# Kernel tuning notes

Hardware: AMD Instinct MI355X
Metric: run time of the kernel (lower is better)

## Reference

```python
import jax, jax.numpy as jnp
import numpy as np

D = 512        # latent_dim
DT = 256       # text_latent_dim
H = 8          # num_heads
TE = 2048      # time_embed_dim
NEG = -1000000.0


def _ln(x, g, b, eps=1e-5):
    m = jnp.mean(x, axis=-1, keepdims=True)
    v = jnp.mean(jnp.square(x - m), axis=-1, keepdims=True)
    return (x - m) * jax.lax.rsqrt(v + eps) * g + b


def _linear(x, W, b):
    return x @ W.T + b


def setup_inputs() -> dict:
    key = jax.random.key(0)
    ks = jax.random.split(key, 24)
    B, T, NT, R, LR = 32, 1024, 77, 4, 256
    inp = {
        'x': jax.random.normal(ks[0], (B, T, D), jnp.float32),
        'xf': jax.random.normal(ks[1], (B, NT, DT), jnp.float32),
        'emb': jax.random.normal(ks[2], (B, TE), jnp.float32),
        'src_mask': jax.random.randint(ks[3], (B, T, 1), 0, 2).astype(jnp.float32),
        'cond_type': jax.random.randint(ks[4], (B, 1, 1), 0, 100).astype(jnp.int32),
        're_motion': jax.random.normal(ks[5], (B, R, LR, D), jnp.float32),
        're_text': jax.random.normal(ks[6], (B, R, 1, D), jnp.float32),
        're_mask': jax.random.randint(ks[7], (B, R, LR), 0, 2).astype(jnp.float32),
    }
    s = 0.02
    def W(k, o, i):
        return jax.random.normal(k, (o, i), jnp.float32) * s
    params = {
        'norm_g': jnp.ones((D,), jnp.float32), 'norm_b': jnp.zeros((D,), jnp.float32),
        'tnorm_g': jnp.ones((DT,), jnp.float32), 'tnorm_b': jnp.zeros((DT,), jnp.float32),
        'rn1_g': jnp.ones((2 * D,), jnp.float32), 'rn1_b': jnp.zeros((2 * D,), jnp.float32),
        'rn2_g': jnp.ones((D,), jnp.float32), 'rn2_b': jnp.zeros((D,), jnp.float32),
        'Wq': W(ks[8], D, D), 'bq': jnp.zeros((D,), jnp.float32),
        'Wkt': W(ks[9], D, DT), 'bkt': jnp.zeros((D,), jnp.float32),
        'Wvt': W(ks[10], D, DT), 'bvt': jnp.zeros((D,), jnp.float32),
        'Wkm': W(ks[11], D, D), 'bkm': jnp.zeros((D,), jnp.float32),
        'Wvm': W(ks[12], D, D), 'bvm': jnp.zeros((D,), jnp.float32),
        'Wkr': W(ks[13], D, 2 * D), 'bkr': jnp.zeros((D,), jnp.float32),
        'Wvr': W(ks[14], D, D), 'bvr': jnp.zeros((D,), jnp.float32),
        'emb_W': W(ks[15], 2 * D, TE), 'emb_b': jnp.zeros((2 * D,), jnp.float32),
        'snorm_g': jnp.ones((D,), jnp.float32), 'snorm_b': jnp.zeros((D,), jnp.float32),
        'out_W': W(ks[16], D, D), 'out_b': jnp.zeros((D,), jnp.float32),
    }
    inp.update(params)
    return inp


def _forward(x, xf, emb, src_mask, cond_type, re_motion, re_text, re_mask,
             norm_g, norm_b, tnorm_g, tnorm_b, rn1_g, rn1_b, rn2_g, rn2_b,
             Wq, bq, Wkt, bkt, Wvt, bvt, Wkm, bkm, Wvm, bvm, Wkr, bkr, Wvr, bvr,
             emb_W, emb_b, snorm_g, snorm_b, out_W, out_b):
    B, T, _ = x.shape
    re_mask_r = re_mask.reshape(B, -1, 1)                       # [B, R*LR, 1]
    N = xf.shape[1] + T + re_motion.shape[1] * re_motion.shape[2]

    xn = _ln(x, norm_g, norm_b)                                  # [B,T,D]
    xfn = _ln(xf, tnorm_g, tnorm_b)                              # [B,NT,DT]
    query = _linear(xn, Wq, bq)                                  # [B,T,D]

    text_ct = (cond_type % 10 > 0).astype(x.dtype)               # [B,1,1]
    retr_ct = (cond_type // 10 > 0).astype(x.dtype)              # [B,1,1]

    re_text_rep = jnp.broadcast_to(re_text, re_motion.shape)     # repeat along Lr
    re_feat_key = jnp.concatenate([re_motion, re_text_rep], axis=-1).reshape(B, -1, 2 * D)

    k_text = _linear(xfn, Wkt, bkt) + (1.0 - text_ct) * NEG
    k_retr = (_linear(_ln(re_feat_key, rn1_g, rn1_b), Wkr, bkr)
              + (1.0 - retr_ct) * NEG + (1.0 - re_mask_r) * NEG)
    k_mot = _linear(xn, Wkm, bkm) + (1.0 - src_mask) * NEG
    key_cat = jnp.concatenate([k_text, k_retr, k_mot], axis=1)   # [B,N,D]

    q = jax.nn.softmax(query.reshape(B, T, H, -1), axis=-1)      # softmax over head_dim
    k = jax.nn.softmax(key_cat.reshape(B, N, H, -1), axis=1)     # softmax over tokens

    re_feat_value = re_motion.reshape(B, -1, D)
    v_text = _linear(xfn, Wvt, bvt) * text_ct
    v_retr = _linear(_ln(re_feat_value, rn2_g, rn2_b), Wvr, bvr) * retr_ct * re_mask_r
    v_mot = _linear(xn, Wvm, bvm) * src_mask
    v = jnp.concatenate([v_text, v_retr, v_mot], axis=1).reshape(B, N, H, -1)

    attention = jnp.einsum('bnhd,bnhl->bhdl', k, v)              # [B,H,hd,hd]
    y = jnp.einsum('bthd,bhdl->bthl', q, attention).reshape(B, T, D)

    # StylizationBlock: film-style scale/shift from time embedding, zero-init out proj
    emb_out = _linear(jax.nn.silu(emb), emb_W, emb_b)[:, None, :]  # [B,1,2D]
    scale, shift = emb_out[..., :D], emb_out[..., D:]
    h = _ln(y, snorm_g, snorm_b) * (1.0 + scale) + shift
    h = _linear(jax.nn.silu(h), out_W, out_b)
    return x + h


def reference(x, xf, emb, src_mask, cond_type, re_motion, re_text, re_mask,
              norm_g, norm_b, tnorm_g, tnorm_b, rn1_g, rn1_b, rn2_g, rn2_b,
              Wq, bq, Wkt, bkt, Wvt, bvt, Wkm, bkm, Wvm, bvm, Wkr, bkr, Wvr, bvr,
              emb_W, emb_b, snorm_g, snorm_b, out_W, out_b):
    return _forward(x, xf, emb, src_mask, cond_type, re_motion, re_text, re_mask,
                    norm_g, norm_b, tnorm_g, tnorm_b, rn1_g, rn1_b, rn2_g, rn2_b,
                    Wq, bq, Wkt, bkt, Wvt, bvt, Wkm, bkm, Wvm, bvm, Wkr, bkr, Wvr, bvr,
                    emb_W, emb_b, snorm_g, snorm_b, out_W, out_b)
```

## Files before the change

### kernel.cpp

```cpp
#include <hip/hip_runtime.h>
#include <cstddef>
#include <cstdint>

#define DEV __device__ __forceinline__

namespace {

constexpr int kH = 8;
constexpr int kB = 32, kT = 1024, kNT = 77, kR = 4, kLR = 256;
constexpr int kRL = kR * kLR;
constexpr int kN = kNT + kRL + kT;
constexpr float kNEG = -1000000.0f;
constexpr int kNS = 8;
constexpr int kSL = 272;
constexpr int kLDSW = 136;

typedef __bf16 bf16x8 __attribute__((ext_vector_type(8)));
typedef float f32x4 __attribute__((ext_vector_type(4)));

DEV unsigned short f2bf(float f) {
  unsigned int u = __float_as_uint(f);
  u += 0x7fffu + ((u >> 16) & 1u);
  return (unsigned short)(u >> 16);
}
DEV float bf2f(unsigned short h) { return __uint_as_float(((unsigned int)h) << 16); }

DEV float wave_sum(float v) {
  #pragma unroll
  for (int s = 32; s; s >>= 1) v += __shfl_xor(v, s);
  return v;
}

template<int COLS>
__global__ __launch_bounds__(256) void ln_bf16(const float* __restrict__ in,
    const float* __restrict__ g, const float* __restrict__ be,
    unsigned short* __restrict__ out) {
  constexpr int PT = COLS / 256;
  int row = blockIdx.x;
  const float* p = in + (size_t)row * COLS;
  unsigned short* o = out + (size_t)row * COLS;
  float v[PT]; float s = 0.f, s2 = 0.f;
  #pragma unroll
  for (int i = 0; i < PT; i++) {
    v[i] = p[threadIdx.x + i * 256];
    s += v[i]; s2 += v[i] * v[i];
  }
  __shared__ float red[2][4];
  int lane = threadIdx.x & 63, w = threadIdx.x >> 6;
  s = wave_sum(s); s2 = wave_sum(s2);
  if (!lane) { red[0][w] = s; red[1][w] = s2; }
  __syncthreads();
  s = red[0][0] + red[0][1] + red[0][2] + red[0][3];
  s2 = red[1][0] + red[1][1] + red[1][2] + red[1][3];
  float mean = s / COLS;
  float var = s2 / COLS - mean * mean;
  float rstd = rsqrtf(var + 1e-5f);
  #pragma unroll
  for (int i = 0; i < PT; i++) {
    int c = threadIdx.x + i * 256;
    o[c] = f2bf((v[i] - mean) * rstd * g[c] + be[c]);
  }
}

__global__ __launch_bounds__(256) void rfk_norm(const float* __restrict__ mot,
    const float* __restrict__ txt,
    const float* __restrict__ g1, const float* __restrict__ b1,
    const float* __restrict__ g2, const float* __restrict__ b2,
    unsigned short* __restrict__ rfk, unsigned short* __restrict__ rfv) {
  int m = blockIdx.x;
  const float* pm = mot + (size_t)m * 512;
  const float* pt = txt + (size_t)(m >> 8) * 512;
  float v[2], t[2];
  float sv = 0.f, sv2 = 0.f, st = 0.f, st2 = 0.f;
  #pragma unroll
  for (int i = 0; i < 2; i++) {
    v[i] = pm[threadIdx.x + i * 256]; sv += v[i]; sv2 += v[i] * v[i];
    t[i] = pt[threadIdx.x + i * 256]; st += t[i]; st2 += t[i] * t[i];
  }
  __shared__ float red[4][4];
  int lane = threadIdx.x & 63, w = threadIdx.x >> 6;
  sv = wave_sum(sv); sv2 = wave_sum(sv2); st = wave_sum(st); st2 = wave_sum(st2);
  if (!lane) { red[0][w] = sv; red[1][w] = sv2; red[2][w] = st; red[3][w] = st2; }
  __syncthreads();
  float SV = red[0][0] + red[0][1] + red[0][2] + red[0][3];
  float SV2 = red[1][0] + red[1][1] + red[1][2] + red[1][3];
  float ST = red[2][0] + red[2][1] + red[2][2] + red[2][3];
  float ST2 = red[3][0] + red[3][1] + red[3][2] + red[3][3];
  float SA = SV + ST, SA2 = SV2 + ST2;
  float ma = SA / 1024.f, va = SA2 / 1024.f - ma * ma;
  float ra_ = rsqrtf(va + 1e-5f);
  float mv = SV / 512.f, vv = SV2 / 512.f - mv * mv;
  float rv_ = rsqrtf(vv + 1e-5f);
  #pragma unroll
  for (int i = 0; i < 2; i++) {
    int c = threadIdx.x + i * 256;
    rfk[(size_t)m * 1024 + c]       = f2bf((v[i] - ma) * ra_ * g1[c] + b1[c]);
    rfk[(size_t)m * 1024 + 512 + c] = f2bf((t[i] - ma) * ra_ * g1[512 + c] + b1[512 + c]);
    rfv[(size_t)m * 512 + c]        = f2bf((v[i] - mv) * rv_ * g2[c] + b2[c]);
  }
}

__global__ __launch_bounds__(256) void rowmask_kernel(const int* __restrict__ ct,
    const float* __restrict__ src_mask, const float* __restrict__ re_mask,
    float* __restrict__ kaT, float* __restrict__ kaR, float* __restrict__ kaM,
    float* __restrict__ vmT, float* __restrict__ vmR, float* __restrict__ vmM,
    int nB) {
  int i = blockIdx.x * 256 + threadIdx.x;
  if (i < nB * kRL) {
    int b = i >> 10;
    int c = ct[b];
    float retr = (c / 10 > 0) ? 1.f : 0.f;
    float rm = re_mask[i];
    kaR[i] = (1.f - retr) * kNEG + (1.f - rm) * kNEG;
    vmR[i] = retr * rm;
    float sm = src_mask[i];
    kaM[i] = (1.f - sm) * kNEG;
    vmM[i] = sm;
  }
  if (i < nB * kNT) {
    int b = i / kNT;
    int c = ct[b];
    float text = (c % 10 > 0) ? 1.f : 0.f;
    kaT[i] = (1.f - text) * kNEG;
    vmT[i] = text;
  }
}

__global__ __launch_bounds__(256) void castw(const float* __restrict__ s,
    unsigned short* __restrict__ d, int n) {
  int i = (blockIdx.x * 256 + threadIdx.x) * 4;
  if (i < n) {
    float4 v = *reinterpret_cast<const float4*>(s + i);
    ushort4 o;
    o.x = f2bf(v.x); o.y = f2bf(v.y); o.z = f2bf(v.z); o.w = f2bf(v.w);
    *reinterpret_cast<ushort4*>(d + i) = o;
  }
}

__global__ __launch_bounds__(256) void silu_emb(const float* __restrict__ emb,
    float* __restrict__ semb) {
  int i = (blockIdx.x * 256 + threadIdx.x) * 4;
  float4 v = *reinterpret_cast<const float4*>(emb + i);
  float4 o;
  o.x = v.x / (1.f + __expf(-v.x));
  o.y = v.y / (1.f + __expf(-v.y));
  o.z = v.z / (1.f + __expf(-v.z));
  o.w = v.w / (1.f + __expf(-v.w));
  *reinterpret_cast<float4*>(semb + i) = o;
}

__global__ __launch_bounds__(256) void emb_gemv2(const float* __restrict__ semb,
    const float* __restrict__ W, float* __restrict__ part) {
  int n = blockIdx.x * 4 + (threadIdx.x >> 6);
  int s = blockIdx.y;
  int lane = threadIdx.x & 63;
  int k = s * 256 + lane * 4;
  float4 wv = *reinterpret_cast<const float4*>(&W[(size_t)n * 2048 + k]);
  float acc[32];
  #pragma unroll
  for (int m = 0; m < 32; m++) {
    float4 sv = *reinterpret_cast<const float4*>(&semb[(size_t)m * 2048 + k]);
    acc[m] = fmaf(sv.x, wv.x, fmaf(sv.y, wv.y, fmaf(sv.z, wv.z, sv.w * wv.w)));
  }
  #pragma unroll
  for (int m = 0; m < 32; m++) {
    float t = wave_sum(acc[m]);
    if (lane == 0) part[((size_t)s * 32 + m) * 1024 + n] = t;
  }
}
__global__ __launch_bounds__(256) void emb_fin(const float* __restrict__ part,
    const float* __restrict__ bias, float* __restrict__ ss) {
  int i = blockIdx.x * 256 + threadIdx.x;
  float s = 0.f;
  #pragma unroll
  for (int c = 0; c < 8; c++) s += part[(size_t)c * 32768 + i];
  ss[i] = s + bias[i & 1023];
}

template<int OUTMODE>
__global__ __launch_bounds__(256) void gemm_mfma(
    const unsigned short* __restrict__ A, const unsigned short* __restrict__ W,
    const float* __restrict__ bias, void* __restrict__ Cout,
    int M, int K, int m_per_b, int n_total, int out_off,
    const float* __restrict__ rowAdd, const float* __restrict__ rowMul,
    const float* __restrict__ addX) {
  __shared__ __align__(16) char smem[34816];
  unsigned short* lds = (unsigned short*)smem;
  const int tid = threadIdx.x;
  const int lane = tid & 63;
  const int wv = tid >> 6;
  const int wr = (wv >> 1) * 64;
  const int wc = (wv & 1) * 64;
  const int m0 = blockIdx.y * 128;
  const int n0 = blockIdx.x * 128;

  const unsigned short* srcA[2]; const unsigned short* srcB[2];
  int dstOff[2];
  #pragma unroll
  for (int i = 0; i < 2; i++) {
    int lin = i * 256 + tid;
    int r = lin >> 2, cl = lin & 3;
    int cs = cl ^ ((r >> 1) & 3);
    int ra = m0 + r; if (ra > M - 1) ra = M - 1;
    srcA[i] = A + (size_t)ra * K + cs * 8;
    srcB[i] = W + (size_t)(n0 + r) * K + cs * 8;
    dstOff[i] = lin * 8;
  }
  int offA[4], offB[4];
  #pragma unroll
  for (int i = 0; i < 4; i++) {
    int r = wr + i * 16 + (lane & 15);
    int c = (lane >> 4) ^ ((r >> 1) & 3);
    offA[i] = r * 32 + c * 8;
    int rb = wc + i * 16 + (lane & 15);
    int cb = (lane >> 4) ^ ((rb >> 1) & 3);
    offB[i] = rb * 32 + cb * 8;
  }

  f32x4 acc[4][4] = {};

  #pragma unroll
  for (int i = 0; i < 2; i++) {
    __builtin_amdgcn_global_load_lds(
        (const __attribute__((address_space(1))) void*)(srcA[i]),
        (__attribute__((address_space(3))) void*)&lds[dstOff[i]], 16, 0, 0);
    __builtin_amdgcn_global_load_lds(
        (const __attribute__((address_space(1))) void*)(srcB[i]),
        (__attribute__((address_space(3))) void*)&lds[4096 + dstOff[i]], 16, 0, 0);
  }
  __syncthreads();

  int c = 0;
  for (int k0 = 0; k0 < K; k0 += 32) {
    int nc = c ^ 1;
    if (k0 + 32 < K) {
      #pragma unroll
      for (int i = 0; i < 2; i++) {
        __builtin_amdgcn_global_load_lds(
            (const __attribute__((address_space(1))) void*)(srcA[i] + k0 + 32),
            (__attribute__((address_space(3))) void*)&lds[nc * 8192 + dstOff[i]], 16, 0, 0);
        __builtin_amdgcn_global_load_lds(
            (const __attribute__((address_space(1))) void*)(srcB[i] + k0 + 32),
            (__attribute__((address_space(3))) void*)&lds[nc * 8192 + 4096 + dstOff[i]], 16, 0, 0);
      }
    }
    bf16x8 af[4], bf[4];
    #pragma unroll
    for (int i = 0; i < 4; i++) {
      af[i] = *reinterpret_cast<const bf16x8*>(&lds[c * 8192 + offA[i]]);
      bf[i] = *reinterpret_cast<const bf16x8*>(&lds[c * 8192 + 4096 + offB[i]]);
    }
    #pragma unroll
    for (int i = 0; i < 4; i++)
      #pragma unroll
      for (int j = 0; j < 4; j++)
        acc[i][j] = __builtin_amdgcn_mfma_f32_16x16x32_bf16(af[i], bf[j], acc[i][j], 0, 0, 0);
    __syncthreads();
    c = nc;
  }

  const int r4 = (lane >> 4) << 2;
  if (OUTMODE != 0) {
    unsigned short* S = (unsigned short*)smem;
    #pragma unroll
    for (int i = 0; i < 4; i++) {
      #pragma unroll
      for (int r = 0; r < 4; r++) {
        int row_t = wr + i * 16 + r4 + r;
        int rowg = m0 + row_t; if (rowg > M - 1) rowg = M - 1;
        float ra = rowAdd ? rowAdd[rowg] : 0.f;
        float rm = rowMul ? rowMul[rowg] : 1.f;
        #pragma unroll
        for (int j = 0; j < 4; j++) {
          int col_t = wc + j * 16 + (lane & 15);
          float v = (acc[i][j][r] + bias[n0 + col_t] + ra) * rm;
          if (OUTMODE == 2) v = __expf(v);
          S[row_t * kLDSW + col_t] = f2bf(v);
        }
      }
    }
    __syncthreads();
    #pragma unroll
    for (int it = 0; it < 8; it++) {
      int slot = it * 256 + tid;
      int row_t = slot >> 4;
      int cs = (slot & 15) * 8;
      int row = m0 + row_t;
      if (row < M) {
        size_t orow = (size_t)(row / m_per_b) * n_total + out_off + (row % m_per_b);
        ulonglong2 d = *reinterpret_cast<const ulonglong2*>(&S[row_t * kLDSW + cs]);
        *reinterpret_cast<ulonglong2*>((unsigned short*)Cout + orow * 512 + n0 + cs) = d;
      }
    }
  } else {
    float* Sf = (float*)smem;
    #pragma unroll
    for (int p = 0; p < 2; p++) {
      __syncthreads();
      #pragma unroll
      for (int i2 = 0; i2 < 2; i2++) {
        int i = p * 2 + i2;
        #pragma unroll
        for (int r = 0; r < 4; r++) {
          int row_t = wr + i * 16 + r4 + r;
          int srow = (row_t & 31) + ((row_t >> 6) << 5);
          int rowg = m0 + row_t; if (rowg > M - 1) rowg = M - 1;
          float ra = rowAdd ? rowAdd[rowg] : 0.f;
          float rm = rowMul ? rowMul[rowg] : 1.f;
          #pragma unroll
          for (int j = 0; j < 4; j++) {
            int col_t = wc + j * 16 + (lane & 15);
            Sf[srow * kLDSW + col_t] = (acc[i][j][r] + bias[n0 + col_t] + ra) * rm;
          }
        }
      }
      __syncthreads();
      #pragma unroll
      for (int it = 0; it < 8; it++) {
        int slot = it * 256 + tid;
        int srow = slot >> 5;
        int c4 = (slot & 31) * 4;
        int row_t = (srow & 31) + p * 32 + ((srow >> 5) << 6);
        int row = m0 + row_t;
        if (row < M) {
          size_t orow = (size_t)(row / m_per_b) * n_total + out_off + (row % m_per_b);
          float4 v = *reinterpret_cast<const float4*>(&Sf[srow * kLDSW + c4]);
          if (addX) {
            float4 xv = *reinterpret_cast<const float4*>(&addX[(size_t)row * 512 + n0 + c4]);
            v.x += xv.x; v.y += xv.y; v.z += xv.z; v.w += xv.w;
          }
          *reinterpret_cast<float4*>((float*)Cout + orow * 512 + n0 + c4) = v;
        }
      }
    }
  }
}

__global__ __launch_bounds__(256) void attp_kernel(const unsigned short* __restrict__ E,
    const unsigned short* __restrict__ V, float* __restrict__ part,
    float* __restrict__ part_cs) {
  int bh = blockIdx.x; int b = bh >> 3, h = bh & 7;
  int s = blockIdx.y;
  int nbeg = s * kSL;
  int nend = min(kN, nbeg + kSL);
  const unsigned short* Ep = E + (size_t)b * kN * 512 + h * 64;
  const unsigned short* Vp = V + (size_t)b * kN * 512 + h * 64;
  __shared__ __align__(16) char smem[32768];
  unsigned short* Elds = (unsigned short*)smem;
  unsigned short* Vlds = (unsigned short*)(smem + 16384);
  int tid = threadIdx.x, lane = tid & 63, wv = tid >> 6;
  int srow = tid >> 3;
  int sc = tid & 7;
  int cd = tid & 63;
  int cq = tid >> 6;
  f32x4 acc[4][4] = {};
  float csum = 0.f;

  for (int it = 0; it < 3; it++) {
    int tile = nbeg + it * 128;
    __syncthreads();
    #pragma unroll
    for (int r = 0; r < 4; r++) {
      int nl = r * 32 + srow;
      int n = tile + nl;
      ulonglong2 ev, vv;
      ev.x = 0; ev.y = 0; vv.x = 0; vv.y = 0;
      if (n < nend) {
        ev = *reinterpret_cast<const ulonglong2*>(Ep + (size_t)n * 512 + sc * 8);
        vv = *reinterpret_cast<const ulonglong2*>(Vp + (size_t)n * 512 + sc * 8);
      }
      int cp = (sc ^ (nl & 7) ^ ((nl >> 3) & 7)) * 8;
      *reinterpret_cast<ulonglong2*>(&Elds[nl * 64 + cp]) = ev;
      *reinterpret_cast<ulonglong2*>(&Vlds[nl * 64 + cp]) = vv;
    }
    __syncthreads();
    int nf = wv * 32 + ((lane >> 4) << 3);
    int key = (nf >> 3) & 7;
    bf16x8 af[4], bf[4];
    #pragma unroll
    for (int f = 0; f < 4; f++) {
      int d = f * 16 + (lane & 15);
      int cb = (((d >> 3) ^ key) << 3) | (d & 7);
      union { unsigned short u[8]; bf16x8 v; } ra, rb;
      #pragma unroll
      for (int e = 0; e < 8; e++) {
        int off = (nf + e) * 64 + (cb ^ (e << 3));
        ra.u[e] = Elds[off];
        rb.u[e] = Vlds[off];
      }
      af[f] = ra.v; bf[f] = rb.v;
    }
    #pragma unroll
    for (int i = 0; i < 4; i++)
      #pragma unroll
      for (int j = 0; j < 4; j++)
        acc[i][j] = __builtin_amdgcn_mfma_f32_16x16x32_bf16(af[i], bf[j], acc[i][j], 0, 0, 0);
    #pragma unroll
    for (int nn = 0; nn < 32; nn++) {
      int nl = cq * 32 + nn;
      csum += bf2f(Elds[nl * 64 + (((((cd >> 3) ^ (nl & 7) ^ ((nl >> 3) & 7))) << 3) | (cd & 7))]);
    }
  }
  __syncthreads();
  float* attL = (float*)smem;
  float* csu  = (float*)(smem + 17024);
  csu[cq * 64 + cd] = csum;
  for (int p = 0; p < 4; p++) {
    if (wv == p) {
      #pragma unroll
      for (int i = 0; i < 4; i++)
        #pragma unroll
        for (int j = 0; j < 4; j++)
          #pragma unroll
          for (int r = 0; r < 4; r++) {
            int d = i * 16 + ((lane >> 4) << 2) + r;
            int cl = j * 16 + (lane & 15);
            if (p == 0) attL[d * 66 + cl] = acc[i][j][r];
            else        attL[d * 66 + cl] += acc[i][j][r];
          }
    }
    __syncthreads();
  }
  float* op = part + ((size_t)bh * kNS + s) * 4096;
  for (int i = tid; i < 4096; i += 256)
    op[i] = attL[(i >> 6) * 66 + (i & 63)];
  if (tid < 64)
    part_cs[((size_t)bh * kNS + s) * 64 + tid] =
        csu[tid] + csu[64 + tid] + csu[128 + tid] + csu[192 + tid];
}

__global__ __launch_bounds__(256) void attc_kernel(const float* __restrict__ part,
    const float* __restrict__ part_cs, unsigned short* __restrict__ attT) {
  int bh = blockIdx.x;
  __shared__ float at[64][65];
  __shared__ float sinv[64];
  int tid = threadIdx.x;
  if (tid < 64) {
    float s = 0.f;
    #pragma unroll
    for (int c = 0; c < kNS; c++) s += part_cs[((size_t)bh * kNS + c) * 64 + tid];
    sinv[tid] = 1.f / s;
  }
  for (int i = tid; i < 4096; i += 256) {
    float s = 0.f;
    #pragma unroll
    for (int c = 0; c < kNS; c++) s += part[((size_t)bh * kNS + c) * 4096 + i];
    at[i >> 6][i & 63] = s;
  }
  __syncthreads();
  for (int j = tid; j < 4096; j += 256) {
    int l = j >> 6, d = j & 63;
    attT[(size_t)bh * 4096 + j] = f2bf(at[d][l] * sinv[d]);
  }
}

__global__ __launch_bounds__(256) void y_mfma(const unsigned short* __restrict__ q,
    const unsigned short* __restrict__ attT, unsigned short* __restrict__ y) {
  int bh = blockIdx.x; int b = bh >> 3, h = bh & 7;
  int t0 = blockIdx.y * 128;
  __shared__ unsigned short bt[64][72];
  __shared__ float rs[128];
  __shared__ unsigned short ob[128][72];
  int tid = threadIdx.x, lane = tid & 63, wv = tid >> 6;
  int wr = wv * 32;
  for (int i = tid; i < 512; i += 256) {
    int row = i >> 3, c8 = (i & 7) * 8;
    *reinterpret_cast<ulonglong2*>(&bt[row][c8]) =
        *reinterpret_cast<const ulonglong2*>(attT + (size_t)bh * 4096 + row * 64 + c8);
  }
  const unsigned short* qp = q + ((size_t)(b * 1024 + t0 + wr)) * 512 + h * 64;
  bf16x8 af[2][2];
  #pragma unroll
  for (int i = 0; i < 2; i++) {
    int row = i * 16 + (lane & 15);
    #pragma unroll
    for (int s = 0; s < 2; s++)
      af[i][s] = *reinterpret_cast<const bf16x8*>(qp + (size_t)row * 512 + s * 32 + (lane >> 4) * 8);
  }
  #pragma unroll
  for (int i = 0; i < 2; i++) {
    float r = 0.f;
    #pragma unroll
    for (int s = 0; s < 2; s++) {
      const unsigned short* pu = reinterpret_cast<const unsigned short*>(&af[i][s]);
      #pragma unroll
      for (int e = 0; e < 8; e++) r += bf2f(pu[e]);
    }
    r += __shfl_xor(r, 16); r += __shfl_xor(r, 32);
    if (lane < 16) rs[wr + i * 16 + lane] = r;
  }
  __syncthreads();
  f32x4 acc[2][4] = {};
  #pragma unroll
  for (int s = 0; s < 2; s++) {
    #pragma unroll
    for (int j = 0; j < 4; j++) {
      bf16x8 bf = *reinterpret_cast<const bf16x8*>(&bt[j * 16 + (lane & 15)][s * 32 + (lane >> 4) * 8]);
      #pragma unroll
      for (int i = 0; i < 2; i++)
        acc[i][j] = __builtin_amdgcn_mfma_f32_16x16x32_bf16(af[i][s], bf, acc[i][j], 0, 0, 0);
    }
  }
  int r4 = (lane >> 4) << 2;
  #pragma unroll
  for (int i = 0; i < 2; i++) {
    #pragma unroll
    for (int r = 0; r < 4; r++) {
      int row = wr + i * 16 + r4 + r;
      float rinv = 1.f / rs[row];
      #pragma unroll
      for (int j = 0; j < 4; j++)
        ob[row][j * 16 + (lane & 15)] = f2bf(acc[i][j][r] * rinv);
    }
  }
  __syncthreads();
  for (int i = tid; i < 1024; i += 256) {
    int row = i >> 3, c8 = (i & 7) * 8;
    *reinterpret_cast<ulonglong2*>(y + ((size_t)(b * 1024 + t0 + row)) * 512 + h * 64 + c8) =
        *reinterpret_cast<const ulonglong2*>(&ob[row][c8]);
  }
}

__global__ __launch_bounds__(256) void mod_kernel(const unsigned short* __restrict__ y,
    const float* __restrict__ ss, const float* __restrict__ g, const float* __restrict__ be,
    unsigned short* __restrict__ h) {
  int row = blockIdx.x; int b = row >> 10;
  const unsigned short* p = y + (size_t)row * 512;
  unsigned short* o = h + (size_t)row * 512;
  float v[2]; float s = 0.f, s2 = 0.f;
  #pragma unroll
  for (int i = 0; i < 2; i++) {
    v[i] = bf2f(p[threadIdx.x + i * 256]);
    s += v[i]; s2 += v[i] * v[i];
  }
  __shared__ float red[2][4];
  int lane = threadIdx.x & 63, w = threadIdx.x >> 6;
  s = wave_sum(s); s2 = wave_sum(s2);
  if (!lane) { red[0][w] = s; red[1][w] = s2; }
  __syncthreads();
  s = red[0][0] + red[0][1] + red[0][2] + red[0][3];
  s2 = red[1][0] + red[1][1] + red[1][2] + red[1][3];
  float mean = s / 512.f, var = s2 / 512.f - mean * mean;
  float rstd = rsqrtf(var + 1e-5f);
  #pragma unroll
  for (int i = 0; i < 2; i++) {
    int c = threadIdx.x + i * 256;
    float val = (v[i] - mean) * rstd * g[c] + be[c];
    val = val * (1.f + ss[b * 1024 + c]) + ss[b * 1024 + 512 + c];
    o[c] = f2bf(val / (1.f + __expf(-val)));
  }
}

}

extern "C" void kernel_launch(void* const* d_in, const int* in_sizes, int n_in,
                              void* d_out, int out_size, void* d_ws, size_t ws_size,
                              hipStream_t stream) {
  const float* x        = (const float*)d_in[0];
  const float* xf       = (const float*)d_in[1];
  const float* emb      = (const float*)d_in[2];
  const float* src_mask = (const float*)d_in[3];
  const int*   cond     = (const int*)d_in[4];
  const float* re_motion= (const float*)d_in[5];
  const float* re_text  = (const float*)d_in[6];
  const float* re_mask  = (const float*)d_in[7];
  const float* norm_g = (const float*)d_in[8],  * norm_b = (const float*)d_in[9];
  const float* tnorm_g= (const float*)d_in[10], * tnorm_b= (const float*)d_in[11];
  const float* rn1_g  = (const float*)d_in[12], * rn1_b  = (const float*)d_in[13];
  const float* rn2_g  = (const float*)d_in[14], * rn2_b  = (const float*)d_in[15];
  const float* Wq  = (const float*)d_in[16], * bq  = (const float*)d_in[17];
  const float* Wkt = (const float*)d_in[18], * bkt = (const float*)d_in[19];
  const float* Wvt = (const float*)d_in[20], * bvt = (const float*)d_in[21];
  const float* Wkm = (const float*)d_in[22], * bkm = (const float*)d_in[23];
  const float* Wvm = (const float*)d_in[24], * bvm = (const float*)d_in[25];
  const float* Wkr = (const float*)d_in[26], * bkr = (const float*)d_in[27];
  const float* Wvr = (const float*)d_in[28], * bvr = (const float*)d_in[29];
  const float* emb_W = (const float*)d_in[30], * emb_b = (const float*)d_in[31];
  const float* snorm_g = (const float*)d_in[32], * snorm_b = (const float*)d_in[33];
  const float* out_W = (const float*)d_in[34], * out_b = (const float*)d_in[35];
  float* out = (float*)d_out;

  char* base = (char*)d_ws;
  size_t off = 0;
  auto ab = [&](size_t nb) { char* p = base + off; off = (off + nb + 255) & ~(size_t)255; return p; };

  unsigned short* wq_bf  = (unsigned short*)ab(512 * 512 * 2);
  unsigned short* wkt_bf = (unsigned short*)ab(512 * 256 * 2);
  unsigned short* wvt_bf = (unsigned short*)ab(512 * 256 * 2);
  unsigned short* wkm_bf = (unsigned short*)ab(512 * 512 * 2);
  unsigned short* wvm_bf = (unsigned short*)ab(512 * 512 * 2);
  unsigned short* wkr_bf = (unsigned short*)ab(512 * 1024 * 2);
  unsigned short* wvr_bf = (unsigned short*)ab(512 * 512 * 2);
  unsigned short* wout_bf= (unsigned short*)ab(512 * 512 * 2);
  float* semb_f   = (float*)ab((size_t)kB * 2048 * 4);
  float* part_emb = (float*)ab((size_t)8 * kB * 1024 * 4);
  float* ssb_full = (float*)ab((size_t)kB * 1024 * 4);
  float* kaT_full = (float*)ab((size_t)kB * kNT * 4);
  float* vmT_full = (float*)ab((size_t)kB * kNT * 4);
  float* kaR_full = (float*)ab((size_t)kB * kRL * 4);
  float* kaM_full = (float*)ab((size_t)kB * kT * 4);
  float* vmR_full = (float*)ab((size_t)kB * kRL * 4);
  float* vmM_full = (float*)ab((size_t)kB * kT * 4);
  const size_t fixed_off = off;

  auto pad = [](size_t n) { return (n + 255) & ~(size_t)255; };
  auto chunk_bytes = [&](size_t CH) -> size_t {
    size_t s = 0;
    s += pad(CH * 1024 * 512 * 2);
    s += pad(CH * kNT * 256 * 2);
    s += pad(CH * 1024 * 1024 * 2);
    s += pad(CH * 1024 * 512 * 2);
    s += pad(CH * 1024 * 512 * 2);
    s += pad((size_t)CH * kN * 512 * 2);
    s += pad((size_t)CH * kN * 512 * 2);
    s += pad(CH * 8 * 4096 * 2);
    s += pad(CH * 8 * (size_t)kNS * 4096 * 4);
    s += pad(CH * 8 * (size_t)kNS * 64 * 4);
    return s;
  };
  int CH = 32;
  while (CH > 1 && fixed_off + chunk_bytes(CH) > ws_size) CH >>= 1;

  auto cl = [&](const float* s, unsigned short* d, int n) {
    castw<<<dim3((n / 4 + 255) / 256), 256, 0, stream>>>(s, d, n);
  };
  cl(Wq,  wq_bf,  512 * 512);
  cl(Wkt, wkt_bf, 512 * 256);
  cl(Wvt, wvt_bf, 512 * 256);
  cl(Wkm, wkm_bf, 512 * 512);
  cl(Wvm, wvm_bf, 512 * 512);
  cl(Wkr, wkr_bf, 512 * 1024);
  cl(Wvr, wvr_bf, 512 * 512);
  cl(out_W, wout_bf, 512 * 512);

  rowmask_kernel<<<dim3(kB * 4), 256, 0, stream>>>(cond, src_mask, re_mask,
      kaT_full, kaR_full, kaM_full, vmT_full, vmR_full, vmM_full, kB);
  silu_emb<<<dim3(kB * 2048 / 1024), 256, 0, stream>>>(emb, semb_f);
  emb_gemv2<<<dim3(256, 8), 256, 0, stream>>>(semb_f, emb_W, part_emb);
  emb_fin<<<dim3(128), 256, 0, stream>>>(part_emb, emb_b, ssb_full);

  for (int b0 = 0; b0 < kB; b0 += CH) {
    off = fixed_off;
    const int MRc = CH * 1024;
    const int MTc = CH * kNT;

    unsigned short* xn_bf  = (unsigned short*)ab((size_t)MRc * 512 * 2);
    unsigned short* xfn_bf = (unsigned short*)ab((size_t)MTc * 256 * 2);
    unsigned short* rfk_bf = (unsigned short*)ab((size_t)MRc * 1024 * 2);
    unsigned short* rfv_bf = (unsigned short*)ab((size_t)MRc * 512 * 2);
    unsigned short* qb_bf  = (unsigned short*)ab((size_t)MRc * 512 * 2);
    unsigned short* kc_bf  = (unsigned short*)ab((size_t)CH * kN * 512 * 2);
    unsigned short* vb_bf  = (unsigned short*)ab((size_t)CH * kN * 512 * 2);
    unsigned short* attT = (unsigned short*)ab((size_t)CH * 8 * 4096 * 2);
    float* attp = (float*)ab((size_t)CH * 8 * kNS * 4096 * 4);
    float* part_cs = (float*)ab((size_t)CH * 8 * kNS * 64 * 4);
    unsigned short* yb16 = rfk_bf;
    unsigned short* h_bf = xn_bf;

    const float* x_c   = x + (size_t)b0 * kT * 512;
    const float* xf_c  = xf + (size_t)b0 * kNT * 256;
    const float* rm_c  = re_motion + (size_t)b0 * kRL * 512;
    const float* rt_c  = re_text + (size_t)b0 * kR * 512;
    float* out_c = out + (size_t)b0 * kT * 512;

    ln_bf16<512><<<dim3(MRc), 256, 0, stream>>>(x_c, norm_g, norm_b, xn_bf);
    ln_bf16<256><<<dim3(MTc), 256, 0, stream>>>(xf_c, tnorm_g, tnorm_b, xfn_bf);
    rfk_norm<<<dim3(MRc), 256, 0, stream>>>(rm_c, rt_c, rn1_g, rn1_b, rn2_g, rn2_b,
                                            rfk_bf, rfv_bf);

    gemm_mfma<2><<<dim3(4, CH * 8), 256, 0, stream>>>(xn_bf, wq_bf, bq, qb_bf,
        MRc, 512, MRc, 0, 0, nullptr, nullptr, nullptr);
    gemm_mfma<2><<<dim3(4, (MTc + 127) / 128), 256, 0, stream>>>(xfn_bf, wkt_bf, bkt, kc_bf,
        MTc, 256, kNT, kN, 0, kaT_full + (size_t)b0 * kNT, nullptr, nullptr);
    gemm_mfma<2><<<dim3(4, CH * 8), 256, 0, stream>>>(rfk_bf, wkr_bf, bkr, kc_bf,
        MRc, 1024, kRL, kN, kNT, kaR_full + (size_t)b0 * kRL, nullptr, nullptr);
    gemm_mfma<2><<<dim3(4, CH * 8), 256, 0, stream>>>(xn_bf, wkm_bf, bkm, kc_bf,
        MRc, 512, kT, kN, kNT + kRL, kaM_full + (size_t)b0 * kT, nullptr, nullptr);
    gemm_mfma<1><<<dim3(4, (MTc + 127) / 128), 256, 0, stream>>>(xfn_bf, wvt_bf, bvt, vb_bf,
        MTc, 256, kNT, kN, 0, nullptr, vmT_full + (size_t)b0 * kNT, nullptr);
    gemm_mfma<1><<<dim3(4, CH * 8), 256, 0, stream>>>(rfv_bf, wvr_bf, bvr, vb_bf,
        MRc, 512, kRL, kN, kNT, nullptr, vmR_full + (size_t)b0 * kRL, nullptr);
    gemm_mfma<1><<<dim3(4, CH * 8), 256, 0, stream>>>(xn_bf, wvm_bf, bvm, vb_bf,
        MRc, 512, kT, kN, kNT + kRL, nullptr, vmM_full + (size_t)b0 * kT, nullptr);

    attp_kernel<<<dim3(CH * 8, kNS), 256, 0, stream>>>(kc_bf, vb_bf, attp, part_cs);
    attc_kernel<<<dim3(CH * 8), 256, 0, stream>>>(attp, part_cs, attT);
    y_mfma<<<dim3(CH * 8, 8), 256, 0, stream>>>(qb_bf, attT, yb16);

    mod_kernel<<<dim3(MRc), 256, 0, stream>>>(yb16, ssb_full + (size_t)b0 * 1024,
                                              snorm_g, snorm_b, h_bf);
    gemm_mfma<0><<<dim3(4, CH * 8), 256, 0, stream>>>(h_bf, wout_bf, out_b, out_c,
        MRc, 512, MRc, 0, 0, nullptr, nullptr, x_c);
  }
}
```

Baseline: 627.6 us.

## Store K/V transposed (feature-major, padded N) so attention loads are contiguous

The K and V projection GEMMs now write their outputs transposed into a [B*512, 2304] layout, using a swizzled LDS transpose in the epilogue, or scattered scalar stores for the text segment whose row count is not a multiple of 8. A new kernel zeroes the padding columns. The attention-partial kernel then loads contiguous 128-wide tiles per feature row and reads MFMA fragments with vector LDS loads instead of 8 scalar gathers, splitting over 9 slices of 256. This targets the scalar LDS gather cost in the attention kernel. In exchange, the GEMM epilogues do strided global writes, and the text segment uses uncoalesced 2-byte stores.

```diff
diff --git a/kernel.cpp b/kernel.cpp
--- a/kernel.cpp
+++ b/kernel.cpp
@@ -11,8 +11,8 @@
 constexpr int kRL = kR * kLR;
 constexpr int kN = kNT + kRL + kT;
 constexpr float kNEG = -1000000.0f;
-constexpr int kNS = 8;
-constexpr int kSL = 272;
+constexpr int kNtot = 2304;
+constexpr int kNS2 = 9;
 constexpr int kLDSW = 136;
 
 typedef __bf16 bf16x8 __attribute__((ext_vector_type(8)));
@@ -137,6 +137,17 @@
   }
 }
 
+__global__ __launch_bounds__(256) void zpad_kernel(unsigned short* __restrict__ E,
+    unsigned short* __restrict__ V, int rows) {
+  int i = blockIdx.x * 256 + threadIdx.x;
+  if (i >= rows * 24) return;
+  int row = i / 24, c = i % 24;
+  size_t off = (size_t)row * kNtot + 2112 + c * 8;
+  ulonglong2 z; z.x = 0; z.y = 0;
+  *reinterpret_cast<ulonglong2*>(E + off) = z;
+  *reinterpret_cast<ulonglong2*>(V + off) = z;
+}
+
 __global__ __launch_bounds__(256) void silu_emb(const float* __restrict__ emb,
     float* __restrict__ semb) {
   int i = (blockIdx.x * 256 + threadIdx.x) * 4;
@@ -177,7 +188,7 @@
   ss[i] = s + bias[i & 1023];
 }
 
-template<int OUTMODE>
+template<int OUTMODE, int TR>
 __global__ __launch_bounds__(256) void gemm_mfma(
     const unsigned short* __restrict__ A, const unsigned short* __restrict__ W,
     const float* __restrict__ bias, void* __restrict__ Cout,
@@ -260,6 +271,33 @@
   }
 
   const int r4 = (lane >> 4) << 2;
+  const int colb = n0 + wc + (lane & 15);
+  const int rowb = m0 + wr + r4;
+
+  if (OUTMODE != 0 && TR && (m_per_b & 7)) {
+    unsigned short* C16 = (unsigned short*)Cout;
+    #pragma unroll
+    for (int i = 0; i < 4; i++) {
+      #pragma unroll
+      for (int r = 0; r < 4; r++) {
+        int row = rowb + i * 16 + r;
+        if (row >= M) continue;
+        float ra = rowAdd ? rowAdd[row] : 0.f;
+        float rm = rowMul ? rowMul[row] : 1.f;
+        size_t nn = out_off + (row % m_per_b);
+        size_t cb = (size_t)(row / m_per_b) * 512;
+        #pragma unroll
+        for (int j = 0; j < 4; j++) {
+          int col = colb + j * 16;
+          float v = (acc[i][j][r] + bias[col] + ra) * rm;
+          if (OUTMODE == 2) v = __expf(v);
+          C16[(cb + col) * kNtot + nn] = f2bf(v);
+        }
+      }
+    }
+    return;
+  }
+
   if (OUTMODE != 0) {
     unsigned short* S = (unsigned short*)smem;
     #pragma unroll
@@ -270,26 +308,46 @@
         int rowg = m0 + row_t; if (rowg > M - 1) rowg = M - 1;
         float ra = rowAdd ? rowAdd[rowg] : 0.f;
         float rm = rowMul ? rowMul[rowg] : 1.f;
+        int key = TR ? (((row_t >> 3) & 7) << 3) : 0;
         #pragma unroll
         for (int j = 0; j < 4; j++) {
           int col_t = wc + j * 16 + (lane & 15);
           float v = (acc[i][j][r] + bias[n0 + col_t] + ra) * rm;
           if (OUTMODE == 2) v = __expf(v);
-          S[row_t * kLDSW + col_t] = f2bf(v);
+          S[row_t * kLDSW + (col_t ^ key)] = f2bf(v);
         }
       }
     }
     __syncthreads();
-    #pragma unroll
-    for (int it = 0; it < 8; it++) {
-      int slot = it * 256 + tid;
-      int row_t = slot >> 4;
-      int cs = (slot & 15) * 8;
-      int row = m0 + row_t;
-      if (row < M) {
-        size_t orow = (size_t)(row / m_per_b) * n_total + out_off + (row % m_per_b);
-        ulonglong2 d = *reinterpret_cast<const ulonglong2*>(&S[row_t * kLDSW + cs]);
-        *reinterpret_cast<ulonglong2*>((unsigned short*)Cout + orow * 512 + n0 + cs) = d;
+    if (TR) {
+      #pragma unroll
+      for (int it = 0; it < 8; it++) {
+        int slot = it * 256 + tid;
+        int col_t = slot >> 4;
+        int mcx = slot & 15;
+        int mc = mcx * 8;
+        int key = (mcx & 7) << 3;
+        union { unsigned short u[8]; ulonglong2 v; } w;
+        #pragma unroll
+        for (int e = 0; e < 8; e++)
+          w.u[e] = S[(mc + e) * kLDSW + (col_t ^ key)];
+        int row = m0 + mc;
+        size_t obase = ((size_t)(row / m_per_b) * 512 + n0 + col_t) * (size_t)kNtot
+                     + out_off + (row % m_per_b);
+        *reinterpret_cast<ulonglong2*>((unsigned short*)Cout + obase) = w.v;
+      }
+    } else {
+      #pragma unroll
+      for (int it = 0; it < 8; it++) {
+        int slot = it * 256 + tid;
+        int row_t = slot >> 4;
+        int cs = (slot & 15) * 8;
+        int row = m0 + row_t;
+        if (row < M) {
+          size_t orow = (size_t)(row / m_per_b) * n_total + out_off + (row % m_per_b);
+          ulonglong2 d = *reinterpret_cast<const ulonglong2*>(&S[row_t * kLDSW + cs]);
+          *reinterpret_cast<ulonglong2*>((unsigned short*)Cout + orow * 512 + n0 + cs) = d;
+        }
       }
     }
   } else {
@@ -339,56 +397,37 @@
 __global__ __launch_bounds__(256) void attp_kernel(const unsigned short* __restrict__ E,
     const unsigned short* __restrict__ V, float* __restrict__ part,
     float* __restrict__ part_cs) {
-  int bh = blockIdx.x; int b = bh >> 3, h = bh & 7;
+  int bh = blockIdx.x;
   int s = blockIdx.y;
-  int nbeg = s * kSL;
-  int nend = min(kN, nbeg + kSL);
-  const unsigned short* Ep = E + (size_t)b * kN * 512 + h * 64;
-  const unsigned short* Vp = V + (size_t)b * kN * 512 + h * 64;
-  __shared__ __align__(16) char smem[32768];
+  const unsigned short* Ep = E + (size_t)bh * 64 * kNtot;
+  const unsigned short* Vp = V + (size_t)bh * 64 * kNtot;
+  __shared__ __align__(16) char smem[34816];
   unsigned short* Elds = (unsigned short*)smem;
-  unsigned short* Vlds = (unsigned short*)(smem + 16384);
+  unsigned short* Vlds = (unsigned short*)(smem + 17408);
   int tid = threadIdx.x, lane = tid & 63, wv = tid >> 6;
-  int srow = tid >> 3;
-  int sc = tid & 7;
-  int cd = tid & 63;
-  int cq = tid >> 6;
   f32x4 acc[4][4] = {};
   float csum = 0.f;
-
-  for (int it = 0; it < 3; it++) {
-    int tile = nbeg + it * 128;
+  int cd = tid & 63, cq = tid >> 6;
+
+  for (int it = 0; it < 2; it++) {
+    int n0 = s * 256 + it * 128;
     __syncthreads();
     #pragma unroll
     for (int r = 0; r < 4; r++) {
-      int nl = r * 32 + srow;
-      int n = tile + nl;
-      ulonglong2 ev, vv;
-      ev.x = 0; ev.y = 0; vv.x = 0; vv.y = 0;
-      if (n < nend) {
-        ev = *reinterpret_cast<const ulonglong2*>(Ep + (size_t)n * 512 + sc * 8);
-        vv = *reinterpret_cast<const ulonglong2*>(Vp + (size_t)n * 512 + sc * 8);
-      }
-      int cp = (sc ^ (nl & 7) ^ ((nl >> 3) & 7)) * 8;
-      *reinterpret_cast<ulonglong2*>(&Elds[nl * 64 + cp]) = ev;
-      *reinterpret_cast<ulonglong2*>(&Vlds[nl * 64 + cp]) = vv;
+      int ch = r * 256 + tid;
+      int d = ch >> 4, off = (ch & 15) * 8;
+      *reinterpret_cast<ulonglong2*>(&Elds[d * 136 + off]) =
+          *reinterpret_cast<const ulonglong2*>(Ep + (size_t)d * kNtot + n0 + off);
+      *reinterpret_cast<ulonglong2*>(&Vlds[d * 136 + off]) =
+          *reinterpret_cast<const ulonglong2*>(Vp + (size_t)d * kNtot + n0 + off);
     }
     __syncthreads();
     int nf = wv * 32 + ((lane >> 4) << 3);
-    int key = (nf >> 3) & 7;
     bf16x8 af[4], bf[4];
     #pragma unroll
     for (int f = 0; f < 4; f++) {
-      int d = f * 16 + (lane & 15);
-      int cb = (((d >> 3) ^ key) << 3) | (d & 7);
-      union { unsigned short u[8]; bf16x8 v; } ra, rb;
-      #pragma unroll
-      for (int e = 0; e < 8; e++) {
-        int off = (nf + e) * 64 + (cb ^ (e << 3));
-        ra.u[e] = Elds[off];
-        rb.u[e] = Vlds[off];
-      }
-      af[f] = ra.v; bf[f] = rb.v;
+      af[f] = *reinterpret_cast<const bf16x8*>(&Elds[(f * 16 + (lane & 15)) * 136 + nf]);
+      bf[f] = *reinterpret_cast<const bf16x8*>(&Vlds[(f * 16 + (lane & 15)) * 136 + nf]);
     }
     #pragma unroll
     for (int i = 0; i < 4; i++)
@@ -396,14 +435,16 @@
       for (int j = 0; j < 4; j++)
         acc[i][j] = __builtin_amdgcn_mfma_f32_16x16x32_bf16(af[i], bf[j], acc[i][j], 0, 0, 0);
     #pragma unroll
-    for (int nn = 0; nn < 32; nn++) {
-      int nl = cq * 32 + nn;
-      csum += bf2f(Elds[nl * 64 + (((((cd >> 3) ^ (nl & 7) ^ ((nl >> 3) & 7))) << 3) | (cd & 7))]);
+    for (int k8 = 0; k8 < 4; k8++) {
+      bf16x8 ev = *reinterpret_cast<const bf16x8*>(&Elds[cd * 136 + cq * 32 + k8 * 8]);
+      const unsigned short* pu = reinterpret_cast<const unsigned short*>(&ev);
+      #pragma unroll
+      for (int e = 0; e < 8; e++) csum += bf2f(pu[e]);
     }
   }
   __syncthreads();
   float* attL = (float*)smem;
-  float* csu  = (float*)(smem + 17024);
+  float* csu  = (float*)(smem + 17408);
   csu[cq * 64 + cd] = csum;
   for (int p = 0; p < 4; p++) {
     if (wv == p) {
@@ -421,11 +462,11 @@
     }
     __syncthreads();
   }
-  float* op = part + ((size_t)bh * kNS + s) * 4096;
+  float* op = part + ((size_t)bh * kNS2 + s) * 4096;
   for (int i = tid; i < 4096; i += 256)
     op[i] = attL[(i >> 6) * 66 + (i & 63)];
   if (tid < 64)
-    part_cs[((size_t)bh * kNS + s) * 64 + tid] =
+    part_cs[((size_t)bh * kNS2 + s) * 64 + tid] =
         csu[tid] + csu[64 + tid] + csu[128 + tid] + csu[192 + tid];
 }
 
@@ -438,13 +479,13 @@
   if (tid < 64) {
     float s = 0.f;
     #pragma unroll
-    for (int c = 0; c < kNS; c++) s += part_cs[((size_t)bh * kNS + c) * 64 + tid];
+    for (int c = 0; c < kNS2; c++) s += part_cs[((size_t)bh * kNS2 + c) * 64 + tid];
     sinv[tid] = 1.f / s;
   }
   for (int i = tid; i < 4096; i += 256) {
     float s = 0.f;
     #pragma unroll
-    for (int c = 0; c < kNS; c++) s += part[((size_t)bh * kNS + c) * 4096 + i];
+    for (int c = 0; c < kNS2; c++) s += part[((size_t)bh * kNS2 + c) * 4096 + i];
     at[i >> 6][i & 63] = s;
   }
   __syncthreads();
@@ -611,11 +652,11 @@
     s += pad(CH * 1024 * 1024 * 2);
     s += pad(CH * 1024 * 512 * 2);
     s += pad(CH * 1024 * 512 * 2);
-    s += pad((size_t)CH * kN * 512 * 2);
-    s += pad((size_t)CH * kN * 512 * 2);
+    s += pad((size_t)CH * 512 * kNtot * 2);
+    s += pad((size_t)CH * 512 * kNtot * 2);
     s += pad(CH * 8 * 4096 * 2);
-    s += pad(CH * 8 * (size_t)kNS * 4096 * 4);
-    s += pad(CH * 8 * (size_t)kNS * 64 * 4);
+    s += pad(CH * 8 * (size_t)kNS2 * 4096 * 4);
+    s += pad(CH * 8 * (size_t)kNS2 * 64 * 4);
     return s;
   };
   int CH = 32;
@@ -649,11 +690,11 @@
     unsigned short* rfk_bf = (unsigned short*)ab((size_t)MRc * 1024 * 2);
     unsigned short* rfv_bf = (unsigned short*)ab((size_t)MRc * 512 * 2);
     unsigned short* qb_bf  = (unsigned short*)ab((size_t)MRc * 512 * 2);
-    unsigned short* kc_bf  = (unsigned short*)ab((size_t)CH * kN * 512 * 2);
-    unsigned short* vb_bf  = (unsigned short*)ab((size_t)CH * kN * 512 * 2);
+    unsigned short* kc_bf  = (unsigned short*)ab((size_t)CH * 512 * kNtot * 2);
+    unsigned short* vb_bf  = (unsigned short*)ab((size_t)CH * 512 * kNtot * 2);
     unsigned short* attT = (unsigned short*)ab((size_t)CH * 8 * 4096 * 2);
-    float* attp = (float*)ab((size_t)CH * 8 * kNS * 4096 * 4);
-    float* part_cs = (float*)ab((size_t)CH * 8 * kNS * 64 * 4);
+    float* attp = (float*)ab((size_t)CH * 8 * kNS2 * 4096 * 4);
+    float* part_cs = (float*)ab((size_t)CH * 8 * kNS2 * 64 * 4);
     unsigned short* yb16 = rfk_bf;
     unsigned short* h_bf = xn_bf;
 
@@ -667,29 +708,30 @@
     ln_bf16<256><<<dim3(MTc), 256, 0, stream>>>(xf_c, tnorm_g, tnorm_b, xfn_bf);
     rfk_norm<<<dim3(MRc), 256, 0, stream>>>(rm_c, rt_c, rn1_g, rn1_b, rn2_g, rn2_b,
                                             rfk_bf, rfv_bf);
-
-    gemm_mfma<2><<<dim3(4, CH * 8), 256, 0, stream>>>(xn_bf, wq_bf, bq, qb_bf,
+    zpad_kernel<<<dim3(CH * 48), 256, 0, stream>>>(kc_bf, vb_bf, CH * 512);
+
+    gemm_mfma<2, 0><<<dim3(4, CH * 8), 256, 0, stream>>>(xn_bf, wq_bf, bq, qb_bf,
         MRc, 512, MRc, 0, 0, nullptr, nullptr, nullptr);
-    gemm_mfma<2><<<dim3(4, (MTc + 127) / 128), 256, 0, stream>>>(xfn_bf, wkt_bf, bkt, kc_bf,
-        MTc, 256, kNT, kN, 0, kaT_full + (size_t)b0 * kNT, nullptr, nullptr);
-    gemm_mfma<2><<<dim3(4, CH * 8), 256, 0, stream>>>(rfk_bf, wkr_bf, bkr, kc_bf,
-        MRc, 1024, kRL, kN, kNT, kaR_full + (size_t)b0 * kRL, nullptr, nullptr);
-    gemm_mfma<2><<<dim3(4, CH * 8), 256, 0, stream>>>(xn_bf, wkm_bf, bkm, kc_bf,
-        MRc, 512, kT, kN, kNT + kRL, kaM_full + (size_t)b0 * kT, nullptr, nullptr);
-    gemm_mfma<1><<<dim3(4, (MTc + 127) / 128), 256, 0, stream>>>(xfn_bf, wvt_bf, bvt, vb_bf,
-        MTc, 256, kNT, kN, 0, nullptr, vmT_full + (size_t)b0 * kNT, nullptr);
-    gemm_mfma<1><<<dim3(4, CH * 8), 256, 0, stream>>>(rfv_bf, wvr_bf, bvr, vb_bf,
-        MRc, 512, kRL, kN, kNT, nullptr, vmR_full + (size_t)b0 * kRL, nullptr);
-    gemm_mfma<1><<<dim3(4, CH * 8), 256, 0, stream>>>(xn_bf, wvm_bf, bvm, vb_bf,
-        MRc, 512, kT, kN, kNT + kRL, nullptr, vmM_full + (size_t)b0 * kT, nullptr);
-
-    attp_kernel<<<dim3(CH * 8, kNS), 256, 0, stream>>>(kc_bf, vb_bf, attp, part_cs);
+    gemm_mfma<2, 1><<<dim3(4, (MTc + 127) / 128), 256, 0, stream>>>(xfn_bf, wkt_bf, bkt, kc_bf,
+        MTc, 256, kNT, 0, 0, kaT_full + (size_t)b0 * kNT, nullptr, nullptr);
+    gemm_mfma<2, 1><<<dim3(4, CH * 8), 256, 0, stream>>>(rfk_bf, wkr_bf, bkr, kc_bf,
+        MRc, 1024, kRL, 0, kNT, kaR_full + (size_t)b0 * kRL, nullptr, nullptr);
+    gemm_mfma<2, 1><<<dim3(4, CH * 8), 256, 0, stream>>>(xn_bf, wkm_bf, bkm, kc_bf,
+        MRc, 512, kT, 0, kNT + kRL, kaM_full + (size_t)b0 * kT, nullptr, nullptr);
+    gemm_mfma<1, 1><<<dim3(4, (MTc + 127) / 128), 256, 0, stream>>>(xfn_bf, wvt_bf, bvt, vb_bf,
+        MTc, 256, kNT, 0, 0, nullptr, vmT_full + (size_t)b0 * kNT, nullptr);
+    gemm_mfma<1, 1><<<dim3(4, CH * 8), 256, 0, stream>>>(rfv_bf, wvr_bf, bvr, vb_bf,
+        MRc, 512, kRL, 0, kNT, nullptr, vmR_full + (size_t)b0 * kRL, nullptr);
+    gemm_mfma<1, 1><<<dim3(4, CH * 8), 256, 0, stream>>>(xn_bf, wvm_bf, bvm, vb_bf,
+        MRc, 512, kT, 0, kNT + kRL, nullptr, vmM_full + (size_t)b0 * kT, nullptr);
+
+    attp_kernel<<<dim3(CH * 8, kNS2), 256, 0, stream>>>(kc_bf, vb_bf, attp, part_cs);
     attc_kernel<<<dim3(CH * 8), 256, 0, stream>>>(attp, part_cs, attT);
     y_mfma<<<dim3(CH * 8, 8), 256, 0, stream>>>(qb_bf, attT, yb16);
 
     mod_kernel<<<dim3(MRc), 256, 0, stream>>>(yb16, ssb_full + (size_t)b0 * 1024,
                                               snorm_g, snorm_b, h_bf);
-    gemm_mfma<0><<<dim3(4, CH * 8), 256, 0, stream>>>(h_bf, wout_bf, out_b, out_c,
+    gemm_mfma<0, 0><<<dim3(4, CH * 8), 256, 0, stream>>>(h_bf, wout_bf, out_b, out_c,
         MRc, 512, MRc, 0, 0, nullptr, nullptr, x_c);
   }
 }
```

New measurement: 641.1 us. 2.2% more time.
